# Performance work log

Measured on AMD Instinct MI355X. Metric: run time of the kernel, lower is better.

## Reference

```python
import jax, jax.numpy as jnp
import numpy as np

T, B, D_IN, HID, D_OUT = 512, 64, 1024, 512, 10


def _gru_dir(x, w_ih, w_hh, b_ih, b_hh, reverse):
    # x: [T,B,D]; w_ih: [3H,D]; w_hh: [3H,H]; biases: [3H]
    xp = jnp.einsum('tbd,gd->tbg', x, w_ih) + b_ih  # [T,B,3H]
    if reverse:
        xp = xp[::-1]
    H = w_hh.shape[1]

    def step(h, xt):
        gh = h @ w_hh.T + b_hh                      # [B,3H]
        xr, xz, xn = jnp.split(xt, 3, axis=-1)
        hr, hz, hn = jnp.split(gh, 3, axis=-1)
        r = jax.nn.sigmoid(xr + hr)
        z = jax.nn.sigmoid(xz + hz)
        n = jnp.tanh(xn + r * hn)
        h_new = (1.0 - z) * n + z * h
        return h_new, h_new

    h0 = jnp.zeros((x.shape[1], H), x.dtype)
    _, hs = jax.lax.scan(step, h0, xp)              # [T,B,H]
    if reverse:
        hs = hs[::-1]
    return hs


def setup_inputs() -> dict:
    key = jax.random.key(0)
    ks = jax.random.split(key, 20)
    k = 1.0 / np.sqrt(HID)
    u = lambda kk, sh, lim: jax.random.uniform(kk, sh, jnp.float32, -lim, lim)
    inp = {
        'numerical': jax.random.normal(ks[0], (B, 8), jnp.float32),
        'embedding': jax.random.normal(ks[1], (T, B, D_IN), jnp.float32),
        # GRU forward direction
        'w_ih_f': u(ks[2], (3 * HID, D_IN), k),
        'w_hh_f': u(ks[3], (3 * HID, HID), k),
        'b_ih_f': u(ks[4], (3 * HID,), k),
        'b_hh_f': u(ks[5], (3 * HID,), k),
        # GRU backward direction
        'w_ih_b': u(ks[6], (3 * HID, D_IN), k),
        'w_hh_b': u(ks[7], (3 * HID, HID), k),
        'b_ih_b': u(ks[8], (3 * HID,), k),
        'b_hh_b': u(ks[9], (3 * HID,), k),
        # attention params (normal std 0.05 per _create_weights)
        'attn_w': 0.05 * jax.random.normal(ks[10], (2 * HID, 2 * HID), jnp.float32),
        'attn_b': 0.05 * jax.random.normal(ks[11], (1, 2 * HID), jnp.float32),
        'ctx_w': 0.05 * jax.random.normal(ks[12], (2 * HID, 1), jnp.float32),
        # classifier: Linear(D_in -> hidden) -> ReLU -> Linear(hidden -> D_out)
        'cls_w1': u(ks[13], (D_IN, HID), 1.0 / np.sqrt(D_IN)),
        'cls_b1': u(ks[14], (HID,), 1.0 / np.sqrt(D_IN)),
        'cls_w2': u(ks[15], (HID, D_OUT), 1.0 / np.sqrt(HID)),
        'cls_b2': u(ks[16], (D_OUT,), 1.0 / np.sqrt(HID)),
    }
    return inp


def reference(numerical, embedding,
              w_ih_f, w_hh_f, b_ih_f, b_hh_f,
              w_ih_b, w_hh_b, b_ih_b, b_hh_b,
              attn_w, attn_b, ctx_w,
              cls_w1, cls_b1, cls_w2, cls_b2):
    # bidirectional GRU: [T,B,2H]
    hf = _gru_dir(embedding, w_ih_f, w_hh_f, b_ih_f, b_hh_f, reverse=False)
    hb = _gru_dir(embedding, w_ih_b, w_hh_b, b_ih_b, b_hh_b, reverse=True)
    f_output = jnp.concatenate([hf, hb], axis=-1)
    # additive attention: tanh(f W + b), then tanh(. @ ctx) -> scores [T,B]
    att = jnp.tanh(jnp.einsum('tbd,de->tbe', f_output, attn_w) + attn_b)
    scores = jnp.tanh(att @ ctx_w)[..., 0]          # [T,B]
    w = jax.nn.softmax(scores.T, axis=1)            # [B,T]
    ctx = jnp.einsum('tbd,bt->bd', f_output, w)     # [B,2H]
    # classifier
    hid = jax.nn.relu(ctx @ cls_w1 + cls_b1)
    out = hid @ cls_w2 + cls_b2                     # [B,D_OUT]
    return out
```

## Files before the change

### kernel.cpp

```cpp
#include <hip/hip_runtime.h>
#include <stdint.h>

#define T_   512
#define B_   64
#define DIN  1024
#define HID  512
#define G3   1536
#define NC   3072
#define MROWS 32768

typedef __bf16 bf16;
typedef __bf16 bf16x8 __attribute__((ext_vector_type(8)));
typedef float  f32x4  __attribute__((ext_vector_type(4)));

#define GLOBAL_AS __attribute__((address_space(1)))
#define LDS_AS    __attribute__((address_space(3)))

#define LDT(p) __hip_atomic_load((p), __ATOMIC_RELAXED, __HIP_MEMORY_SCOPE_AGENT)

__device__ __forceinline__ uint16_t f2bf_bits(float x){
  union{float f; uint32_t u;} v; v.f = x;
  uint32_t u = v.u;
  u += 0x7FFFu + ((u >> 16) & 1u);
  return (uint16_t)(u >> 16);
}
__device__ __forceinline__ float bf2f_bits(uint16_t h){
  union{uint32_t u; float f;} v; v.u = ((uint32_t)h) << 16;
  return v.f;
}
__device__ __forceinline__ float sig_f(float x){
  return 1.f/(1.f + __expf(-x));
}
__device__ __forceinline__ float tanh_f(float x){
  return 1.f - 2.f/(1.f + __expf(2.f*x));
}
__device__ __forceinline__ bf16x8 as_bf16x8(uint4 u){
  union{uint4 a; bf16x8 b;} c; c.a = u; return c.b;
}

__global__ void k_conv_emb(const float* __restrict__ src, uint16_t* __restrict__ dst, long n8){
  long i = (long)blockIdx.x*blockDim.x + threadIdx.x;
  if(i >= n8) return;
  const float4* s = (const float4*)src;
  float4 a = s[i*2], b = s[i*2+1];
  uint32_t p0 = (uint32_t)f2bf_bits(a.x) | ((uint32_t)f2bf_bits(a.y) << 16);
  uint32_t p1 = (uint32_t)f2bf_bits(a.z) | ((uint32_t)f2bf_bits(a.w) << 16);
  uint32_t p2 = (uint32_t)f2bf_bits(b.x) | ((uint32_t)f2bf_bits(b.y) << 16);
  uint32_t p3 = (uint32_t)f2bf_bits(b.z) | ((uint32_t)f2bf_bits(b.w) << 16);
  ((uint4*)dst)[i] = make_uint4(p0,p1,p2,p3);
}

__global__ void k_conv_wcat(const float* __restrict__ wf, const float* __restrict__ wb, uint16_t* __restrict__ dst, int n){
  int i = blockIdx.x*256 + threadIdx.x;
  if(i >= n) return;
  float v = (i < G3*DIN) ? wf[i] : wb[i - G3*DIN];
  dst[i] = f2bf_bits(v);
}

__global__ void k_conv_awt(const float* __restrict__ aw, uint16_t* __restrict__ dst, int n){
  int i = blockIdx.x*256 + threadIdx.x;
  if(i >= n) return;
  int e = i >> 10, d = i & 1023;
  dst[i] = f2bf_bits(aw[d*1024 + e]);
}

__global__ void k_conv_whh(const float* __restrict__ wf, const float* __restrict__ wb, uint4* __restrict__ wmem){
  int idx = blockIdx.x*256 + threadIdx.x;
  if(idx >= 2*16*96*64) return;
  int c  = idx & 63;
  int t2 = idx >> 6;
  int lc = t2 % 96;
  int t3 = t2 / 96;
  int member = t3 & 15, dir = t3 >> 4;
  int ct = lc >> 4, rr = lc & 15;
  int gcol = (ct >> 1)*512 + member*32 + (ct & 1)*16 + rr;
  int csrc = c ^ (lc & 7);
  const float* src = (dir ? wb : wf) + (size_t)gcol*512 + csrc*8;
  float4 f0 = *(const float4*)src;
  float4 f1 = *(const float4*)(src + 4);
  uint32_t p0 = (uint32_t)f2bf_bits(f0.x) | ((uint32_t)f2bf_bits(f0.y) << 16);
  uint32_t p1 = (uint32_t)f2bf_bits(f0.z) | ((uint32_t)f2bf_bits(f0.w) << 16);
  uint32_t p2 = (uint32_t)f2bf_bits(f1.x) | ((uint32_t)f2bf_bits(f1.y) << 16);
  uint32_t p3 = (uint32_t)f2bf_bits(f1.z) | ((uint32_t)f2bf_bits(f1.w) << 16);
  wmem[idx] = make_uint4(p0,p1,p2,p3);
}

__launch_bounds__(256)
__global__ void k_gemm_xp(const uint16_t* __restrict__ A, const uint16_t* __restrict__ Bw,
                          const float* __restrict__ bihf, const float* __restrict__ bihb,
                          uint16_t* __restrict__ C)
{
  __shared__ uint16_t lA[2][128*32];
  __shared__ uint16_t lB[2][128*32];
  const int K = 1024;
  int bn = blockIdx.x, bm = blockIdx.y;
  int tid = threadIdx.x;
  int lane = tid & 63, wid = tid >> 6;
  int wm = wid >> 1, wn = wid & 1;
  int rowBase = bm*128, colBase = bn*128;
  int rg = lane >> 4, rr = lane & 15;

  auto stage = [&](int buf, int kt){
    #pragma unroll
    for(int i=0;i<2;i++){
      int e = (i*256 + tid)*8;
      int r = e >> 5, c = e & 31;
      __builtin_amdgcn_global_load_lds((const GLOBAL_AS void*)(A + (size_t)(rowBase + r)*K + kt*32 + c),
                                       (LDS_AS void*)&lA[buf][e], 16, 0, 0);
    }
    #pragma unroll
    for(int i=0;i<2;i++){
      int e = (i*256 + tid)*8;
      int r = e >> 5, c = e & 31;
      __builtin_amdgcn_global_load_lds((const GLOBAL_AS void*)(Bw + (size_t)(colBase + r)*K + kt*32 + c),
                                       (LDS_AS void*)&lB[buf][e], 16, 0, 0);
    }
  };

  f32x4 acc[4][4];
  #pragma unroll
  for(int mi=0;mi<4;mi++)
    #pragma unroll
    for(int ni=0;ni<4;ni++) acc[mi][ni] = (f32x4){0.f,0.f,0.f,0.f};

  stage(0, 0);
  __syncthreads();
  for(int kt=0; kt<32; kt++){
    int buf = kt & 1;
    if(kt+1 < 32) stage(buf^1, kt+1);
    bf16x8 af[4], bfv[4];
    #pragma unroll
    for(int mi=0;mi<4;mi++)
      af[mi] = *(const bf16x8*)&lA[buf][(wm*64 + mi*16 + rr)*32 + rg*8];
    #pragma unroll
    for(int ni=0;ni<4;ni++)
      bfv[ni] = *(const bf16x8*)&lB[buf][(wn*64 + ni*16 + rr)*32 + rg*8];
    #pragma unroll
    for(int mi=0;mi<4;mi++)
      #pragma unroll
      for(int ni=0;ni<4;ni++)
        acc[mi][ni] = __builtin_amdgcn_mfma_f32_16x16x32_bf16(af[mi], bfv[ni], acc[mi][ni], 0,0,0);
    __syncthreads();
  }

  #pragma unroll
  for(int ni=0;ni<4;ni++){
    int col = colBase + wn*64 + ni*16 + rr;
    float bv = (col < G3) ? bihf[col] : bihb[col - G3];
    int dircol = (col >= G3) ? 1 : 0;
    int cm = col - dircol*G3;
    int g  = cm >> 9;
    int j  = cm & 511;
    int mem = j >> 5, cc = j & 31;
    #pragma unroll
    for(int mi=0;mi<4;mi++){
      int row0 = rowBase + wm*64 + mi*16 + rg*4;
      int tt = row0 >> 6;
      int b0 = row0 & 63;
      int bgx = b0 >> 4, rr0 = b0 & 15;
      size_t ob = (((((size_t)dircol*512 + tt)*4 + bgx)*16 + mem)*3 + g)*512 + rr0*32 + cc;
      C[ob]      = f2bf_bits(acc[mi][ni][0]+bv);
      C[ob+32]   = f2bf_bits(acc[mi][ni][1]+bv);
      C[ob+64]   = f2bf_bits(acc[mi][ni][2]+bv);
      C[ob+96]   = f2bf_bits(acc[mi][ni][3]+bv);
    }
  }
}

__launch_bounds__(256)
__global__ void k_gemm_att(const uint16_t* __restrict__ A, const uint16_t* __restrict__ Bw,
                           const float* __restrict__ attn_b, const float* __restrict__ ctx_w,
                           float* __restrict__ scores_raw)
{
  __shared__ uint16_t lA[2][128*32];
  __shared__ uint16_t lB[2][128*32];
  const int K = 1024;
  int bn = blockIdx.x, bm = blockIdx.y;
  int tid = threadIdx.x;
  int lane = tid & 63, wid = tid >> 6;
  int wm = wid >> 1, wn = wid & 1;
  int rowBase = bm*128, colBase = bn*128;
  int rg = lane >> 4, rr = lane & 15;

  auto stage = [&](int buf, int kt){
    #pragma unroll
    for(int i=0;i<2;i++){
      int e = (i*256 + tid)*8;
      int r = e >> 5, c = e & 31;
      __builtin_amdgcn_global_load_lds((const GLOBAL_AS void*)(A + (size_t)(rowBase + r)*K + kt*32 + c),
                                       (LDS_AS void*)&lA[buf][e], 16, 0, 0);
    }
    #pragma unroll
    for(int i=0;i<2;i++){
      int e = (i*256 + tid)*8;
      int r = e >> 5, c = e & 31;
      __builtin_amdgcn_global_load_lds((const GLOBAL_AS void*)(Bw + (size_t)(colBase + r)*K + kt*32 + c),
                                       (LDS_AS void*)&lB[buf][e], 16, 0, 0);
    }
  };

  f32x4 acc[4][4];
  #pragma unroll
  for(int mi=0;mi<4;mi++)
    #pragma unroll
    for(int ni=0;ni<4;ni++) acc[mi][ni] = (f32x4){0.f,0.f,0.f,0.f};

  stage(0, 0);
  __syncthreads();
  for(int kt=0; kt<32; kt++){
    int buf = kt & 1;
    if(kt+1 < 32) stage(buf^1, kt+1);
    bf16x8 af[4], bfv[4];
    #pragma unroll
    for(int mi=0;mi<4;mi++)
      af[mi] = *(const bf16x8*)&lA[buf][(wm*64 + mi*16 + rr)*32 + rg*8];
    #pragma unroll
    for(int ni=0;ni<4;ni++)
      bfv[ni] = *(const bf16x8*)&lB[buf][(wn*64 + ni*16 + rr)*32 + rg*8];
    #pragma unroll
    for(int mi=0;mi<4;mi++)
      #pragma unroll
      for(int ni=0;ni<4;ni++)
        acc[mi][ni] = __builtin_amdgcn_mfma_f32_16x16x32_bf16(af[mi], bfv[ni], acc[mi][ni], 0,0,0);
    __syncthreads();
  }

  float ab[4], cw[4];
  #pragma unroll
  for(int ni=0;ni<4;ni++){
    int col = colBase + wn*64 + ni*16 + rr;
    ab[ni] = attn_b[col];
    cw[ni] = ctx_w[col];
  }
  #pragma unroll
  for(int mi=0;mi<4;mi++){
    #pragma unroll
    for(int r=0;r<4;r++){
      float part = 0.f;
      #pragma unroll
      for(int ni=0;ni<4;ni++) part += tanhf(acc[mi][ni][r] + ab[ni]) * cw[ni];
      #pragma unroll
      for(int off=1; off<16; off<<=1) part += __shfl_xor(part, off);
      if(rr == 0){
        int row = rowBase + wm*64 + mi*16 + rg*4 + r;
        atomicAdd(&scores_raw[row], part);
      }
    }
  }
}

__launch_bounds__(768, 3)
__global__ void k_recur(const uint16_t* __restrict__ xp,
                        const uint4* __restrict__ wmem,
                        const float* __restrict__ bhhf, const float* __restrict__ bhhb,
                        unsigned long long* __restrict__ tagbuf,
                        uint16_t* __restrict__ f_out)
{
  __shared__ uint16_t hl[16*512];
  __shared__ float    ghl[2*6*16*17];

  int bid = blockIdx.x;
  int dir = bid & 1, bg = (bid >> 1) & 3, member = bid >> 3;
  int jb = member*32;
  int tid = threadIdx.x;
  int lane = tid & 63, w = tid >> 6;
  int rr = lane & 15, rg = lane >> 4;
  int ct = w >> 1, kh = w & 1;

  const uint4* wsl = wmem + (size_t)(dir*16 + member)*6144 + (ct*16 + rr)*64;
  int xm = rr & 7;
  uint4 wu0 = wsl[(kh*32 +  0 + rg) ^ xm];
  uint4 wu1 = wsl[(kh*32 +  4 + rg) ^ xm];
  uint4 wu2 = wsl[(kh*32 +  8 + rg) ^ xm];
  uint4 wu3 = wsl[(kh*32 + 12 + rg) ^ xm];
  uint4 wu4 = wsl[(kh*32 + 16 + rg) ^ xm];
  uint4 wu5 = wsl[(kh*32 + 20 + rg) ^ xm];
  uint4 wu6 = wsl[(kh*32 + 24 + rg) ^ xm];
  uint4 wu7 = wsl[(kh*32 + 28 + rg) ^ xm];
  asm volatile("" :: "v"(wu0.x), "v"(wu0.y), "v"(wu0.z), "v"(wu0.w),
                     "v"(wu1.x), "v"(wu1.y), "v"(wu1.z), "v"(wu1.w));
  asm volatile("" :: "v"(wu2.x), "v"(wu2.y), "v"(wu2.z), "v"(wu2.w),
                     "v"(wu3.x), "v"(wu3.y), "v"(wu3.z), "v"(wu3.w));
  asm volatile("" :: "v"(wu4.x), "v"(wu4.y), "v"(wu4.z), "v"(wu4.w),
                     "v"(wu5.x), "v"(wu5.y), "v"(wu5.z), "v"(wu5.w));
  asm volatile("" :: "v"(wu6.x), "v"(wu6.y), "v"(wu6.z), "v"(wu6.w),
                     "v"(wu7.x), "v"(wu7.y), "v"(wu7.z), "v"(wu7.w));

  for(int i = tid; i < 2*6*16*17; i += 768) ghl[i] = 0.f;

  int gcol = tid & 31;
  const float* bhh = dir ? bhhb : bhhf;
  float bR = 0.f, bZ = 0.f, bN = 0.f, hprev = 0.f;
  if(tid < 512){
    bR = bhh[jb + gcol];
    bZ = bhh[512 + jb + gcol];
    bN = bhh[1024 + jb + gcol];
  }

  int srow = tid >> 5;
  int sbase = tid & 31;
  int cswz = ((sbase >> 2) ^ (srow & 7));
  int lpos0 = srow*512 + cswz*8 + (sbase & 3)*2;

  __syncthreads();

  #pragma unroll 1
  for(int t = 0; t < 512; t++){
    int trow = dir ? (511 - t) : t;

    uint16_t xr16 = 0, xz16 = 0, xn16 = 0;
    if(tid < 512){
      const uint16_t* xb = xp + (((((size_t)dir*512 + trow)*4 + bg)*16 + member)*3)*512;
      xr16 = xb[tid];
      xz16 = xb[512 + tid];
      xn16 = xb[1024 + tid];
    }

    if(t > 0 && tid < 512){
      const unsigned long long* tb =
        tagbuf + ((size_t)((dir*2 + ((t-1) & 1))*4 + bg)*16 + srow)*256 + sbase;
      unsigned want = (unsigned)t;
      unsigned long long v0,v1,v2,v3,v4,v5,v6,v7;
      bool ok;
      do {
        v0 = LDT(tb+0);   v1 = LDT(tb+32);  v2 = LDT(tb+64);  v3 = LDT(tb+96);
        v4 = LDT(tb+128); v5 = LDT(tb+160); v6 = LDT(tb+192); v7 = LDT(tb+224);
        ok = ((unsigned)v0 == want) & ((unsigned)v1 == want)
           & ((unsigned)v2 == want) & ((unsigned)v3 == want)
           & ((unsigned)v4 == want) & ((unsigned)v5 == want)
           & ((unsigned)v6 == want) & ((unsigned)v7 == want);
      } while(!ok);
      *(uint32_t*)&hl[lpos0 +   0] = (uint32_t)(v0 >> 32);
      *(uint32_t*)&hl[lpos0 +  64] = (uint32_t)(v1 >> 32);
      *(uint32_t*)&hl[lpos0 + 128] = (uint32_t)(v2 >> 32);
      *(uint32_t*)&hl[lpos0 + 192] = (uint32_t)(v3 >> 32);
      *(uint32_t*)&hl[lpos0 + 256] = (uint32_t)(v4 >> 32);
      *(uint32_t*)&hl[lpos0 + 320] = (uint32_t)(v5 >> 32);
      *(uint32_t*)&hl[lpos0 + 384] = (uint32_t)(v6 >> 32);
      *(uint32_t*)&hl[lpos0 + 448] = (uint32_t)(v7 >> 32);
    }
    __syncthreads();

    if(t > 0){
      f32x4 acc = (f32x4){0.f,0.f,0.f,0.f};
      {
        bf16x8 a0 = *(const bf16x8*)&hl[rr*512 + ((kh*32 +  0 + rg) ^ xm)*8];
        acc = __builtin_amdgcn_mfma_f32_16x16x32_bf16(a0, as_bf16x8(wu0), acc, 0,0,0);
        bf16x8 a1 = *(const bf16x8*)&hl[rr*512 + ((kh*32 +  4 + rg) ^ xm)*8];
        acc = __builtin_amdgcn_mfma_f32_16x16x32_bf16(a1, as_bf16x8(wu1), acc, 0,0,0);
        bf16x8 a2 = *(const bf16x8*)&hl[rr*512 + ((kh*32 +  8 + rg) ^ xm)*8];
        acc = __builtin_amdgcn_mfma_f32_16x16x32_bf16(a2, as_bf16x8(wu2), acc, 0,0,0);
        bf16x8 a3 = *(const bf16x8*)&hl[rr*512 + ((kh*32 + 12 + rg) ^ xm)*8];
        acc = __builtin_amdgcn_mfma_f32_16x16x32_bf16(a3, as_bf16x8(wu3), acc, 0,0,0);
        bf16x8 a4 = *(const bf16x8*)&hl[rr*512 + ((kh*32 + 16 + rg) ^ xm)*8];
        acc = __builtin_amdgcn_mfma_f32_16x16x32_bf16(a4, as_bf16x8(wu4), acc, 0,0,0);
        bf16x8 a5 = *(const bf16x8*)&hl[rr*512 + ((kh*32 + 20 + rg) ^ xm)*8];
        acc = __builtin_amdgcn_mfma_f32_16x16x32_bf16(a5, as_bf16x8(wu5), acc, 0,0,0);
        bf16x8 a6 = *(const bf16x8*)&hl[rr*512 + ((kh*32 + 24 + rg) ^ xm)*8];
        acc = __builtin_amdgcn_mfma_f32_16x16x32_bf16(a6, as_bf16x8(wu6), acc, 0,0,0);
        bf16x8 a7 = *(const bf16x8*)&hl[rr*512 + ((kh*32 + 28 + rg) ^ xm)*8];
        acc = __builtin_amdgcn_mfma_f32_16x16x32_bf16(a7, as_bf16x8(wu7), acc, 0,0,0);
      }
      #pragma unroll
      for(int j = 0; j < 4; j++)
        ghl[((kh*6 + ct)*16 + rg*4 + j)*17 + rr] = acc[j];
    }
    __syncthreads();

    if(tid < 512){
      int grow = tid >> 5;
      int c16 = gcol >> 4, cc = gcol & 15;
      float gR = ghl[((0 + c16)*16 + grow)*17 + cc] + ghl[((6  + c16)*16 + grow)*17 + cc] + bR;
      float gZ = ghl[((2 + c16)*16 + grow)*17 + cc] + ghl[((8  + c16)*16 + grow)*17 + cc] + bZ;
      float gN = ghl[((4 + c16)*16 + grow)*17 + cc] + ghl[((10 + c16)*16 + grow)*17 + cc] + bN;
      float rv = sig_f(bf2f_bits(xr16) + gR);
      float zv = sig_f(bf2f_bits(xz16) + gZ);
      float nv = tanh_f(bf2f_bits(xn16) + rv*gN);
      float hnew = (1.f - zv)*nv + zv*hprev;
      hprev = hnew;
      unsigned hb = (unsigned)f2bf_bits(hnew);
      unsigned nb = (unsigned)__shfl_down((int)hb, 1);
      if((tid & 1) == 0){
        unsigned pk = hb | (nb << 16);
        int slot = member*16 + (gcol >> 1);
        unsigned long long pv = ((unsigned long long)pk << 32) | (unsigned)(t + 1);
        __hip_atomic_store(
          tagbuf + ((size_t)((dir*2 + (t & 1))*4 + bg)*16 + grow)*256 + slot,
          pv, __ATOMIC_RELAXED, __HIP_MEMORY_SCOPE_AGENT);
        *(unsigned*)&f_out[((size_t)trow*64 + bg*16 + grow)*1024 + dir*512 + jb + gcol] = pk;
      }
    }
  }
}

__global__ void k_softmax(const float* __restrict__ scores_raw, float* __restrict__ wsm){
  __shared__ float sv[512];
  __shared__ float red[8];
  int b = blockIdx.x;
  int tid = threadIdx.x;
  float mymax = -1e30f;
  for(int t = tid; t < 512; t += 256){
    float s = tanhf(scores_raw[t*64 + b]);
    sv[t] = s;
    mymax = fmaxf(mymax, s);
  }
  #pragma unroll
  for(int off=1; off<64; off<<=1) mymax = fmaxf(mymax, __shfl_xor(mymax, off));
  if((tid&63)==0) red[tid>>6] = mymax;
  __syncthreads();
  float bmax = fmaxf(fmaxf(red[0],red[1]), fmaxf(red[2],red[3]));
  __syncthreads();
  float mysum = 0.f;
  for(int t = tid; t < 512; t += 256){
    float e = __expf(sv[t] - bmax);
    sv[t] = e;
    mysum += e;
  }
  #pragma unroll
  for(int off=1; off<64; off<<=1) mysum += __shfl_xor(mysum, off);
  if((tid&63)==0) red[tid>>6] = mysum;
  __syncthreads();
  float inv = 1.f/(red[0]+red[1]+red[2]+red[3]);
  for(int t = tid; t < 512; t += 256) wsm[b*512 + t] = sv[t]*inv;
}

__global__ void k_ctx(const uint16_t* __restrict__ f_out, const float* __restrict__ wsm, float* __restrict__ ctx){
  __shared__ float wloc[512];
  int b = blockIdx.x >> 2, chunk = blockIdx.x & 3;
  int tid = threadIdx.x;
  for(int t = tid; t < 512; t += 256) wloc[t] = wsm[b*512 + t];
  __syncthreads();
  int d = chunk*256 + tid;
  float acc = 0.f;
  #pragma unroll 8
  for(int t = 0; t < 512; t++)
    acc += wloc[t] * bf2f_bits(f_out[(size_t)(t*64 + b)*1024 + d]);
  ctx[b*1024 + d] = acc;
}

__global__ void k_cls1(const float* __restrict__ ctx, const float* __restrict__ w1,
                       const float* __restrict__ b1, float* __restrict__ hid){
  int idx = blockIdx.x*256 + threadIdx.x;
  int b = idx >> 9, h = idx & 511;
  float acc = b1[h];
  for(int d = 0; d < 1024; d++) acc += ctx[b*1024 + d] * w1[d*512 + h];
  hid[idx] = fmaxf(acc, 0.f);
}

__global__ void k_cls2(const float* __restrict__ hid, const float* __restrict__ w2,
                       const float* __restrict__ b2, float* __restrict__ out){
  int idx = blockIdx.x;
  int b = idx / 10, o = idx % 10;
  int lane = threadIdx.x;
  float acc = 0.f;
  #pragma unroll
  for(int k = 0; k < 8; k++){
    int h = lane + k*64;
    acc += hid[b*512 + h] * w2[h*10 + o];
  }
  #pragma unroll
  for(int off = 1; off < 64; off <<= 1) acc += __shfl_xor(acc, off);
  if(lane == 0) out[idx] = acc + b2[o];
}

extern "C" void kernel_launch(void* const* d_in, const int* in_sizes, int n_in,
                              void* d_out, int out_size, void* d_ws, size_t ws_size,
                              hipStream_t stream)
{
  const float* emb    = (const float*)d_in[1];
  const float* w_ih_f = (const float*)d_in[2];
  const float* w_hh_f = (const float*)d_in[3];
  const float* b_ih_f = (const float*)d_in[4];
  const float* b_hh_f = (const float*)d_in[5];
  const float* w_ih_b = (const float*)d_in[6];
  const float* w_hh_b = (const float*)d_in[7];
  const float* b_ih_b = (const float*)d_in[8];
  const float* b_hh_b = (const float*)d_in[9];
  const float* attn_w = (const float*)d_in[10];
  const float* attn_b = (const float*)d_in[11];
  const float* ctx_w  = (const float*)d_in[12];
  const float* cls_w1 = (const float*)d_in[13];
  const float* cls_b1 = (const float*)d_in[14];
  const float* cls_w2 = (const float*)d_in[15];
  const float* cls_b2 = (const float*)d_in[16];
  float* out = (float*)d_out;

  char* ws = (char*)d_ws;
  size_t off = 0;
  auto alloc = [&](size_t bytes){ void* p = ws + off; off += (bytes + 255) & ~(size_t)255; return p; };
  uint16_t* femb = (uint16_t*)alloc((size_t)MROWS*DIN*2);
  uint16_t* wcat = (uint16_t*)alloc((size_t)NC*DIN*2);
  uint16_t* xp   = (uint16_t*)alloc((size_t)MROWS*NC*2);
  uint16_t* awT  = (uint16_t*)alloc((size_t)1024*1024*2);
  uint4*    wmem = (uint4*)alloc((size_t)2*16*96*64*16);
  unsigned long long* tagbuf = (unsigned long long*)alloc((size_t)2*2*4*16*256*8);
  float* scraw   = (float*)alloc((size_t)MROWS*4);
  float* wsm     = (float*)alloc((size_t)B_*T_*4);
  float* ctx     = (float*)alloc((size_t)B_*1024*4);
  float* hid     = (float*)alloc((size_t)B_*512*4);

  (void)hipMemsetAsync(tagbuf, 0, (size_t)2*2*4*16*256*8, stream);
  (void)hipMemsetAsync(scraw, 0, (size_t)MROWS*4, stream);

  k_conv_emb<<<16384, 256, 0, stream>>>(emb, femb, (long)MROWS*DIN/8);
  k_conv_wcat<<<12288, 256, 0, stream>>>(w_ih_f, w_ih_b, wcat, NC*DIN);
  k_conv_awt<<<4096, 256, 0, stream>>>(attn_w, awT, 1024*1024);
  k_conv_whh<<<768, 256, 0, stream>>>(w_hh_f, w_hh_b, wmem);

  k_gemm_xp<<<dim3(24,256), 256, 0, stream>>>(femb, wcat, b_ih_f, b_ih_b, xp);

  k_recur<<<128, 768, 0, stream>>>(xp, wmem, b_hh_f, b_hh_b, tagbuf, femb );

  k_gemm_att<<<dim3(8,256), 256, 0, stream>>>(femb, awT, attn_b, ctx_w, scraw);
  k_softmax<<<64, 256, 0, stream>>>(scraw, wsm);
  k_ctx<<<256, 256, 0, stream>>>(femb, wsm, ctx);
  k_cls1<<<128, 256, 0, stream>>>(ctx, cls_w1, cls_b1, hid);
  k_cls2<<<640, 64, 0, stream>>>(hid, cls_w2, cls_b2, out);
}
```

Baseline: 1.499 ms.

## Fuse input-projection GEMM into recurrence kernel with per-timestep readiness counters

Merges the xp input-projection GEMM and the GRU recurrence into one persistent launch. The first 128 blocks run the recurrence, and the rest compute GEMM tiles ordered from both ends of the time axis. Each GEMM tile stages its output through LDS, stores it with coalesced atomic writes and bumps a per-row-block counter. The recurrence spins on that counter before consuming each timestep, so it can start before the whole GEMM finishes. The risks are that GEMM blocks now run with 768 threads but only 256 active, which may cut GEMM occupancy. The recurrence may also stall if those blocks are not scheduled in time, or deadlock if they cannot be.

```diff
diff --git a/kernel.cpp b/kernel.cpp
--- a/kernel.cpp
+++ b/kernel.cpp
@@ -8,6 +8,7 @@
 #define G3   1536
 #define NC   3072
 #define MROWS 32768
+#define RWGS 128
 
 typedef __bf16 bf16;
 typedef __bf16 bf16x8 __attribute__((ext_vector_type(8)));
@@ -16,7 +17,8 @@
 #define GLOBAL_AS __attribute__((address_space(1)))
 #define LDS_AS    __attribute__((address_space(3)))
 
-#define LDT(p) __hip_atomic_load((p), __ATOMIC_RELAXED, __HIP_MEMORY_SCOPE_AGENT)
+#define LDT(p)   __hip_atomic_load((p), __ATOMIC_RELAXED, __HIP_MEMORY_SCOPE_AGENT)
+#define LDT32(p) __hip_atomic_load((p), __ATOMIC_RELAXED, __HIP_MEMORY_SCOPE_AGENT)
 
 __device__ __forceinline__ uint16_t f2bf_bits(float x){
   union{float f; uint32_t u;} v; v.f = x;
@@ -85,184 +87,125 @@
   wmem[idx] = make_uint4(p0,p1,p2,p3);
 }
 
-__launch_bounds__(256)
-__global__ void k_gemm_xp(const uint16_t* __restrict__ A, const uint16_t* __restrict__ Bw,
-                          const float* __restrict__ bihf, const float* __restrict__ bihb,
-                          uint16_t* __restrict__ C)
+__global__ __launch_bounds__(768)
+void k_fused(const uint16_t* __restrict__ A, const uint16_t* __restrict__ Bw,
+             const float* __restrict__ bihf, const float* __restrict__ bihb,
+             uint16_t* __restrict__ xp, unsigned* __restrict__ xctr,
+             const uint4* __restrict__ wmem,
+             const float* __restrict__ bhhf, const float* __restrict__ bhhb,
+             unsigned long long* __restrict__ tagbuf,
+             uint16_t* __restrict__ f_out)
 {
-  __shared__ uint16_t lA[2][128*32];
-  __shared__ uint16_t lB[2][128*32];
-  const int K = 1024;
-  int bn = blockIdx.x, bm = blockIdx.y;
+  __shared__ __align__(16) uint16_t smem[16384];
   int tid = threadIdx.x;
-  int lane = tid & 63, wid = tid >> 6;
-  int wm = wid >> 1, wn = wid & 1;
-  int rowBase = bm*128, colBase = bn*128;
-  int rg = lane >> 4, rr = lane & 15;
-
-  auto stage = [&](int buf, int kt){
-    #pragma unroll
-    for(int i=0;i<2;i++){
-      int e = (i*256 + tid)*8;
-      int r = e >> 5, c = e & 31;
-      __builtin_amdgcn_global_load_lds((const GLOBAL_AS void*)(A + (size_t)(rowBase + r)*K + kt*32 + c),
-                                       (LDS_AS void*)&lA[buf][e], 16, 0, 0);
-    }
-    #pragma unroll
-    for(int i=0;i<2;i++){
-      int e = (i*256 + tid)*8;
-      int r = e >> 5, c = e & 31;
-      __builtin_amdgcn_global_load_lds((const GLOBAL_AS void*)(Bw + (size_t)(colBase + r)*K + kt*32 + c),
-                                       (LDS_AS void*)&lB[buf][e], 16, 0, 0);
-    }
-  };
-
-  f32x4 acc[4][4];
-  #pragma unroll
-  for(int mi=0;mi<4;mi++)
-    #pragma unroll
-    for(int ni=0;ni<4;ni++) acc[mi][ni] = (f32x4){0.f,0.f,0.f,0.f};
-
-  stage(0, 0);
-  __syncthreads();
-  for(int kt=0; kt<32; kt++){
-    int buf = kt & 1;
-    if(kt+1 < 32) stage(buf^1, kt+1);
-    bf16x8 af[4], bfv[4];
+
+  if(blockIdx.x >= RWGS){
+    const int K = 1024;
+    int g = blockIdx.x - RWGS;
+    int bn = g % 24;
+    int i  = g / 24;
+    int bm = (i & 1) ? (255 - (i >> 1)) : (i >> 1);
+    int lane = tid & 63, wid = tid >> 6;
+    int wm = wid >> 1, wn = wid & 1;
+    int rowBase = bm*128, colBase = bn*128;
+    int rg = lane >> 4, rr = lane & 15;
+
+    auto stage = [&](int buf, int kt){
+      if(tid < 256){
+        #pragma unroll
+        for(int i2=0;i2<2;i2++){
+          int e = (i2*256 + tid)*8;
+          int r = e >> 5, c = e & 31;
+          __builtin_amdgcn_global_load_lds((const GLOBAL_AS void*)(A + (size_t)(rowBase + r)*K + kt*32 + c),
+                                           (LDS_AS void*)&smem[buf*4096 + e], 16, 0, 0);
+        }
+        #pragma unroll
+        for(int i2=0;i2<2;i2++){
+          int e = (i2*256 + tid)*8;
+          int r = e >> 5, c = e & 31;
+          __builtin_amdgcn_global_load_lds((const GLOBAL_AS void*)(Bw + (size_t)(colBase + r)*K + kt*32 + c),
+                                           (LDS_AS void*)&smem[8192 + buf*4096 + e], 16, 0, 0);
+        }
+      }
+    };
+
+    f32x4 acc[4][4];
     #pragma unroll
     for(int mi=0;mi<4;mi++)
-      af[mi] = *(const bf16x8*)&lA[buf][(wm*64 + mi*16 + rr)*32 + rg*8];
-    #pragma unroll
-    for(int ni=0;ni<4;ni++)
-      bfv[ni] = *(const bf16x8*)&lB[buf][(wn*64 + ni*16 + rr)*32 + rg*8];
-    #pragma unroll
-    for(int mi=0;mi<4;mi++)
-      #pragma unroll
-      for(int ni=0;ni<4;ni++)
-        acc[mi][ni] = __builtin_amdgcn_mfma_f32_16x16x32_bf16(af[mi], bfv[ni], acc[mi][ni], 0,0,0);
+      #pragma unroll
+      for(int ni=0;ni<4;ni++) acc[mi][ni] = (f32x4){0.f,0.f,0.f,0.f};
+
+    stage(0, 0);
     __syncthreads();
-  }
-
-  #pragma unroll
-  for(int ni=0;ni<4;ni++){
-    int col = colBase + wn*64 + ni*16 + rr;
-    float bv = (col < G3) ? bihf[col] : bihb[col - G3];
-    int dircol = (col >= G3) ? 1 : 0;
-    int cm = col - dircol*G3;
-    int g  = cm >> 9;
-    int j  = cm & 511;
-    int mem = j >> 5, cc = j & 31;
-    #pragma unroll
-    for(int mi=0;mi<4;mi++){
-      int row0 = rowBase + wm*64 + mi*16 + rg*4;
-      int tt = row0 >> 6;
-      int b0 = row0 & 63;
-      int bgx = b0 >> 4, rr0 = b0 & 15;
-      size_t ob = (((((size_t)dircol*512 + tt)*4 + bgx)*16 + mem)*3 + g)*512 + rr0*32 + cc;
-      C[ob]      = f2bf_bits(acc[mi][ni][0]+bv);
-      C[ob+32]   = f2bf_bits(acc[mi][ni][1]+bv);
-      C[ob+64]   = f2bf_bits(acc[mi][ni][2]+bv);
-      C[ob+96]   = f2bf_bits(acc[mi][ni][3]+bv);
-    }
-  }
-}
-
-__launch_bounds__(256)
-__global__ void k_gemm_att(const uint16_t* __restrict__ A, const uint16_t* __restrict__ Bw,
-                           const float* __restrict__ attn_b, const float* __restrict__ ctx_w,
-                           float* __restrict__ scores_raw)
-{
-  __shared__ uint16_t lA[2][128*32];
-  __shared__ uint16_t lB[2][128*32];
-  const int K = 1024;
-  int bn = blockIdx.x, bm = blockIdx.y;
-  int tid = threadIdx.x;
-  int lane = tid & 63, wid = tid >> 6;
-  int wm = wid >> 1, wn = wid & 1;
-  int rowBase = bm*128, colBase = bn*128;
-  int rg = lane >> 4, rr = lane & 15;
-
-  auto stage = [&](int buf, int kt){
-    #pragma unroll
-    for(int i=0;i<2;i++){
-      int e = (i*256 + tid)*8;
-      int r = e >> 5, c = e & 31;
-      __builtin_amdgcn_global_load_lds((const GLOBAL_AS void*)(A + (size_t)(rowBase + r)*K + kt*32 + c),
-                                       (LDS_AS void*)&lA[buf][e], 16, 0, 0);
-    }
-    #pragma unroll
-    for(int i=0;i<2;i++){
-      int e = (i*256 + tid)*8;
-      int r = e >> 5, c = e & 31;
-      __builtin_amdgcn_global_load_lds((const GLOBAL_AS void*)(Bw + (size_t)(colBase + r)*K + kt*32 + c),
-                                       (LDS_AS void*)&lB[buf][e], 16, 0, 0);
-    }
-  };
-
-  f32x4 acc[4][4];
-  #pragma unroll
-  for(int mi=0;mi<4;mi++)
-    #pragma unroll
-    for(int ni=0;ni<4;ni++) acc[mi][ni] = (f32x4){0.f,0.f,0.f,0.f};
-
-  stage(0, 0);
-  __syncthreads();
-  for(int kt=0; kt<32; kt++){
-    int buf = kt & 1;
-    if(kt+1 < 32) stage(buf^1, kt+1);
-    bf16x8 af[4], bfv[4];
-    #pragma unroll
-    for(int mi=0;mi<4;mi++)
-      af[mi] = *(const bf16x8*)&lA[buf][(wm*64 + mi*16 + rr)*32 + rg*8];
-    #pragma unroll
-    for(int ni=0;ni<4;ni++)
-      bfv[ni] = *(const bf16x8*)&lB[buf][(wn*64 + ni*16 + rr)*32 + rg*8];
-    #pragma unroll
-    for(int mi=0;mi<4;mi++)
-      #pragma unroll
-      for(int ni=0;ni<4;ni++)
-        acc[mi][ni] = __builtin_amdgcn_mfma_f32_16x16x32_bf16(af[mi], bfv[ni], acc[mi][ni], 0,0,0);
+    for(int kt=0; kt<32; kt++){
+      int buf = kt & 1;
+      if(kt+1 < 32) stage(buf^1, kt+1);
+      if(tid < 256){
+        bf16x8 af[4], bfv[4];
+        #pragma unroll
+        for(int mi=0;mi<4;mi++)
+          af[mi] = *(const bf16x8*)&smem[buf*4096 + (wm*64 + mi*16 + rr)*32 + rg*8];
+        #pragma unroll
+        for(int ni=0;ni<4;ni++)
+          bfv[ni] = *(const bf16x8*)&smem[8192 + buf*4096 + (wn*64 + ni*16 + rr)*32 + rg*8];
+        #pragma unroll
+        for(int mi=0;mi<4;mi++)
+          #pragma unroll
+          for(int ni=0;ni<4;ni++)
+            acc[mi][ni] = __builtin_amdgcn_mfma_f32_16x16x32_bf16(af[mi], bfv[ni], acc[mi][ni], 0,0,0);
+      }
+      __syncthreads();
+    }
+
+    if(tid < 256){
+      #pragma unroll
+      for(int ni=0;ni<4;ni++){
+        int col = colBase + wn*64 + ni*16 + rr;
+        float bv = (col < G3) ? bihf[col] : bihb[col - G3];
+        int lc = wn*64 + ni*16 + rr;
+        #pragma unroll
+        for(int mi=0;mi<4;mi++){
+          int row = wm*64 + mi*16 + rg*4;
+          #pragma unroll
+          for(int r=0;r<4;r++)
+            smem[(row+r)*128 + lc] = f2bf_bits(acc[mi][ni][r] + bv);
+        }
+      }
+    }
     __syncthreads();
-  }
-
-  float ab[4], cw[4];
-  #pragma unroll
-  for(int ni=0;ni<4;ni++){
-    int col = colBase + wn*64 + ni*16 + rr;
-    ab[ni] = attn_b[col];
-    cw[ni] = ctx_w[col];
-  }
-  #pragma unroll
-  for(int mi=0;mi<4;mi++){
-    #pragma unroll
-    for(int r=0;r<4;r++){
-      float part = 0.f;
-      #pragma unroll
-      for(int ni=0;ni<4;ni++) part += tanhf(acc[mi][ni][r] + ab[ni]) * cw[ni];
-      #pragma unroll
-      for(int off=1; off<16; off<<=1) part += __shfl_xor(part, off);
-      if(rr == 0){
-        int row = rowBase + wm*64 + mi*16 + rg*4 + r;
-        atomicAdd(&scores_raw[row], part);
-      }
-    }
-  }
-}
-
-__launch_bounds__(768, 3)
-__global__ void k_recur(const uint16_t* __restrict__ xp,
-                        const uint4* __restrict__ wmem,
-                        const float* __restrict__ bhhf, const float* __restrict__ bhhb,
-                        unsigned long long* __restrict__ tagbuf,
-                        uint16_t* __restrict__ f_out)
-{
-  __shared__ uint16_t hl[16*512];
-  __shared__ float    ghl[2*6*16*17];
+
+    int dircol = (colBase >= G3) ? 1 : 0;
+    int cm0 = colBase - dircol*G3;
+    int gg  = cm0 >> 9;
+    int mem0 = (cm0 & 511) >> 5;
+    if(tid < 512){
+      #pragma unroll
+      for(int k=0;k<8;k++){
+        int v = tid*8 + k;
+        int chunk = v >> 7;
+        int off = v & 127;
+        int tt_l = chunk >> 4, bgx = (chunk >> 2) & 3, mem_l = chunk & 3;
+        int row16 = off >> 3, cq = off & 7;
+        int lrow = tt_l*64 + bgx*16 + row16;
+        int lcol = mem_l*32 + cq*4;
+        unsigned long long val = *(const unsigned long long*)&smem[lrow*128 + lcol];
+        size_t cb = ((((size_t)(dircol*512 + 2*bm + tt_l)*4 + bgx)*16 + (mem0 + mem_l))*3 + gg)*512;
+        __hip_atomic_store((unsigned long long*)(xp + cb) + off, val,
+                           __ATOMIC_RELAXED, __HIP_MEMORY_SCOPE_AGENT);
+      }
+    }
+    __syncthreads();
+    if(tid == 0)
+      __hip_atomic_fetch_add(&xctr[bm], 1u, __ATOMIC_RELAXED, __HIP_MEMORY_SCOPE_AGENT);
+    return;
+  }
+
+  uint16_t* hl = smem;
+  float*    ghl = (float*)(smem + 8192);
 
   int bid = blockIdx.x;
   int dir = bid & 1, bg = (bid >> 1) & 3, member = bid >> 3;
   int jb = member*32;
-  int tid = threadIdx.x;
   int lane = tid & 63, w = tid >> 6;
   int rr = lane & 15, rg = lane >> 4;
   int ct = w >> 1, kh = w & 1;
@@ -304,9 +247,21 @@
 
   __syncthreads();
 
+  {
+    int p0 = (dir ? 511 : 0) >> 1;
+    while(LDT32(&xctr[p0]) < 24u) __builtin_amdgcn_s_sleep(2);
+  }
+
   #pragma unroll 1
   for(int t = 0; t < 512; t++){
     int trow = dir ? (511 - t) : t;
+
+    unsigned xc = 24u;
+    int pnext = -1;
+    if(t + 2 < 512){
+      pnext = (dir ? (511 - (t + 2)) : (t + 2)) >> 1;
+      xc = LDT32(&xctr[pnext]);
+    }
 
     uint16_t xr16 = 0, xz16 = 0, xn16 = 0;
     if(tid < 512){
@@ -390,6 +345,94 @@
         *(unsigned*)&f_out[((size_t)trow*64 + bg*16 + grow)*1024 + dir*512 + jb + gcol] = pk;
       }
     }
+    if(pnext >= 0){
+      while(xc < 24u){
+        __builtin_amdgcn_s_sleep(1);
+        xc = LDT32(&xctr[pnext]);
+      }
+    }
+  }
+}
+
+__launch_bounds__(256)
+__global__ void k_gemm_att(const uint16_t* __restrict__ A, const uint16_t* __restrict__ Bw,
+                           const float* __restrict__ attn_b, const float* __restrict__ ctx_w,
+                           float* __restrict__ scores_raw)
+{
+  __shared__ uint16_t lA[2][128*32];
+  __shared__ uint16_t lB[2][128*32];
+  const int K = 1024;
+  int bn = blockIdx.x, bm = blockIdx.y;
+  int tid = threadIdx.x;
+  int lane = tid & 63, wid = tid >> 6;
+  int wm = wid >> 1, wn = wid & 1;
+  int rowBase = bm*128, colBase = bn*128;
+  int rg = lane >> 4, rr = lane & 15;
+
+  auto stage = [&](int buf, int kt){
+    #pragma unroll
+    for(int i=0;i<2;i++){
+      int e = (i*256 + tid)*8;
+      int r = e >> 5, c = e & 31;
+      __builtin_amdgcn_global_load_lds((const GLOBAL_AS void*)(A + (size_t)(rowBase + r)*K + kt*32 + c),
+                                       (LDS_AS void*)&lA[buf][e], 16, 0, 0);
+    }
+    #pragma unroll
+    for(int i=0;i<2;i++){
+      int e = (i*256 + tid)*8;
+      int r = e >> 5, c = e & 31;
+      __builtin_amdgcn_global_load_lds((const GLOBAL_AS void*)(Bw + (size_t)(colBase + r)*K + kt*32 + c),
+                                       (LDS_AS void*)&lB[buf][e], 16, 0, 0);
+    }
+  };
+
+  f32x4 acc[4][4];
+  #pragma unroll
+  for(int mi=0;mi<4;mi++)
+    #pragma unroll
+    for(int ni=0;ni<4;ni++) acc[mi][ni] = (f32x4){0.f,0.f,0.f,0.f};
+
+  stage(0, 0);
+  __syncthreads();
+  for(int kt=0; kt<32; kt++){
+    int buf = kt & 1;
+    if(kt+1 < 32) stage(buf^1, kt+1);
+    bf16x8 af[4], bfv[4];
+    #pragma unroll
+    for(int mi=0;mi<4;mi++)
+      af[mi] = *(const bf16x8*)&lA[buf][(wm*64 + mi*16 + rr)*32 + rg*8];
+    #pragma unroll
+    for(int ni=0;ni<4;ni++)
+      bfv[ni] = *(const bf16x8*)&lB[buf][(wn*64 + ni*16 + rr)*32 + rg*8];
+    #pragma unroll
+    for(int mi=0;mi<4;mi++)
+      #pragma unroll
+      for(int ni=0;ni<4;ni++)
+        acc[mi][ni] = __builtin_amdgcn_mfma_f32_16x16x32_bf16(af[mi], bfv[ni], acc[mi][ni], 0,0,0);
+    __syncthreads();
+  }
+
+  float ab[4], cw[4];
+  #pragma unroll
+  for(int ni=0;ni<4;ni++){
+    int col = colBase + wn*64 + ni*16 + rr;
+    ab[ni] = attn_b[col];
+    cw[ni] = ctx_w[col];
+  }
+  #pragma unroll
+  for(int mi=0;mi<4;mi++){
+    #pragma unroll
+    for(int r=0;r<4;r++){
+      float part = 0.f;
+      #pragma unroll
+      for(int ni=0;ni<4;ni++) part += tanhf(acc[mi][ni][r] + ab[ni]) * cw[ni];
+      #pragma unroll
+      for(int off=1; off<16; off<<=1) part += __shfl_xor(part, off);
+      if(rr == 0){
+        int row = rowBase + wm*64 + mi*16 + rg*4 + r;
+        atomicAdd(&scores_raw[row], part);
+      }
+    }
   }
 }
 
@@ -494,12 +537,14 @@
   uint16_t* awT  = (uint16_t*)alloc((size_t)1024*1024*2);
   uint4*    wmem = (uint4*)alloc((size_t)2*16*96*64*16);
   unsigned long long* tagbuf = (unsigned long long*)alloc((size_t)2*2*4*16*256*8);
+  unsigned* xctr = (unsigned*)alloc(1024);
   float* scraw   = (float*)alloc((size_t)MROWS*4);
   float* wsm     = (float*)alloc((size_t)B_*T_*4);
   float* ctx     = (float*)alloc((size_t)B_*1024*4);
   float* hid     = (float*)alloc((size_t)B_*512*4);
 
   (void)hipMemsetAsync(tagbuf, 0, (size_t)2*2*4*16*256*8, stream);
+  (void)hipMemsetAsync(xctr, 0, 1024, stream);
   (void)hipMemsetAsync(scraw, 0, (size_t)MROWS*4, stream);
 
   k_conv_emb<<<16384, 256, 0, stream>>>(emb, femb, (long)MROWS*DIN/8);
@@ -507,9 +552,9 @@
   k_conv_awt<<<4096, 256, 0, stream>>>(attn_w, awT, 1024*1024);
   k_conv_whh<<<768, 256, 0, stream>>>(w_hh_f, w_hh_b, wmem);
 
-  k_gemm_xp<<<dim3(24,256), 256, 0, stream>>>(femb, wcat, b_ih_f, b_ih_b, xp);
-
-  k_recur<<<128, 768, 0, stream>>>(xp, wmem, b_hh_f, b_hh_b, tagbuf, femb );
+  k_fused<<<RWGS + 24*256, 768, 0, stream>>>(femb, wcat, b_ih_f, b_ih_b,
+                                             xp, xctr, wmem, b_hh_f, b_hh_b,
+                                             tagbuf, femb );
 
   k_gemm_att<<<dim3(8,256), 256, 0, stream>>>(femb, awT, attn_b, ctx_w, scraw);
   k_softmax<<<64, 256, 0, stream>>>(scraw, wsm);
```

New measurement: 1.789 ms. +19.4%, slower.
